# Optimization experiments

Hardware: AMD Instinct MI355X
Metric: run time of the kernel (lower is better)

The kernel has to match this reference:

```python
import jax, jax.numpy as jnp
import numpy as np

PRE_HEIGHT = 96
PRE_WIDTH = 128


def setup_inputs() -> dict:
    key = jax.random.key(0)
    B, K, H, W = 32, 64, 96, 128
    x = jax.random.normal(key, (B, K, H, W), dtype=jnp.float32)
    return {"combined_hm_preds": x, "batch_size": B, "num_of_kp": K}


def reference(combined_hm_preds, batch_size, num_of_kp):
    B, K, H, W = combined_hm_preds.shape
    # nn.Softmax() with no dim on a 4D tensor -> softmax over dim=1 (channels)
    map_val_all = jax.nn.softmax(combined_hm_preds, axis=1)
    # zeta[b,k] = sum over spatial of the channel-softmaxed map
    get_zeta = map_val_all.sum(axis=(2, 3))  # [B, K]
    js = jnp.arange(W, dtype=map_val_all.dtype)
    iis = jnp.arange(H, dtype=map_val_all.dtype)
    # per-channel weighted coordinate sums
    Sx = jnp.einsum('bkij,j->bk', map_val_all, js)  # [B, K]
    Sy = jnp.einsum('bkij,i->bk', map_val_all, iis)  # [B, K]
    # faithful to the original: accumulators are never reset across k or b,
    # so each keypoint uses the inclusive cumulative sum in flattened (b,k) order
    cum_x = jnp.cumsum(Sx.reshape(-1)).reshape(B, K)
    cum_y = jnp.cumsum(Sy.reshape(-1)).reshape(B, K)
    kx = jnp.round(cum_x / get_zeta)
    ky = jnp.round(cum_y / get_zeta)
    # out-of-range clamp to the image center, as in the original
    kx = jnp.where((kx > PRE_WIDTH) | (kx < 0), PRE_WIDTH * 0.5, kx)
    ky = jnp.where((ky > PRE_HEIGHT) | (ky < 0), PRE_HEIGHT * 0.5, ky)
    keypoint = jnp.stack([kx, ky], axis=-1)  # [B, K, 2]
    return (map_val_all, keypoint, get_zeta)
```

## Files before the change

### kernel.cpp

```cpp
#include <hip/hip_runtime.h>
#include <math.h>

#define BB 32
#define KK 64
#define HH 96
#define WW 128
#define HW (HH*WW)
#define MAP_SIZE (BB*KK*HW)
#define NBK (BB*KK)
#define NT  (HW/256)

__global__ __launch_bounds__(256) void fused_k(const float* __restrict__ x,
                                               float* __restrict__ out,
                                               double* __restrict__ sxyz) {
    __shared__ float  sm[KK][257];
    __shared__ float  dinv[256];
    __shared__ double pz[4][64], px[4][64], py[4][64];

    int blk  = blockIdx.x;
    int b    = blk / NT;
    int tile = blk - b * NT;
    int t    = threadIdx.x;
    size_t base = (size_t)b * KK * HW + (size_t)tile * 256 + t;

    float den = 0.f;
    #pragma unroll
    for (int k = 0; k < KK; ++k) {
        float e = __expf(x[base + (size_t)k * HW]);
        sm[k][t] = e;
        den += e;
    }
    float inv = 1.f / den;
    dinv[t] = inv;

    #pragma unroll
    for (int k = 0; k < KK; ++k) {
        out[base + (size_t)k * HW] = sm[k][t] * inv;
    }

    __syncthreads();

    int k = t & 63, chunk = t >> 6;
    int p0 = chunk * 64;
    double z = 0.0, sx = 0.0, sy = 0.0;
    #pragma unroll
    for (int j = 0; j < 64; ++j) {
        int p = p0 + j;
        double m = (double)(sm[k][p] * dinv[p]);
        int g = tile * 256 + p;
        z  += m;
        sx += m * (double)(g & (WW - 1));
        sy += m * (double)(g >> 7);
    }
    pz[chunk][k] = z; px[chunk][k] = sx; py[chunk][k] = sy;
    __syncthreads();

    if (t < 64) {
        double Z  = pz[0][t] + pz[1][t] + pz[2][t] + pz[3][t];
        double SX = px[0][t] + px[1][t] + px[2][t] + px[3][t];
        double SY = py[0][t] + py[1][t] + py[2][t] + py[3][t];
        int bk = b * KK + t;
        atomicAdd(&sxyz[bk * 3 + 0], SX);
        atomicAdd(&sxyz[bk * 3 + 1], SY);
        atomicAdd(&sxyz[bk * 3 + 2], Z);
    }
}

__global__ __launch_bounds__(256) void keypoint_k(const double* __restrict__ sxyz,
                                                  float* __restrict__ kp,
                                                  float* __restrict__ zeta) {
    const int PT = NBK / 256;
    int t = threadIdx.x;
    int lane = t & 63, wid = t >> 6;

    double vx[PT], vy[PT];
    double cx = 0.0, cy = 0.0;
    #pragma unroll
    for (int e = 0; e < PT; ++e) {
        int idx = t * PT + e;
        cx += sxyz[idx * 3 + 0]; vx[e] = cx;
        cy += sxyz[idx * 3 + 1]; vy[e] = cy;
    }
    double tx = cx, ty = cy;
    for (int off = 1; off < 64; off <<= 1) {
        double ax = __shfl_up(tx, off, 64);
        double ay = __shfl_up(ty, off, 64);
        if (lane >= off) { tx += ax; ty += ay; }
    }
    __shared__ double wxs[4], wys[4];
    if (lane == 63) { wxs[wid] = tx; wys[wid] = ty; }
    __syncthreads();
    double offx = tx - cx, offy = ty - cy;
    for (int w2 = 0; w2 < wid; ++w2) { offx += wxs[w2]; offy += wys[w2]; }

    #pragma unroll
    for (int e = 0; e < PT; ++e) {
        int idx = t * PT + e;
        double zz = sxyz[idx * 3 + 2];
        double kx = rint((vx[e] + offx) / zz);
        double ky = rint((vy[e] + offy) / zz);
        float fkx = (float)kx, fky = (float)ky;
        if (fkx > 128.0f || fkx < 0.0f) fkx = 64.0f;
        if (fky > 96.0f  || fky < 0.0f) fky = 48.0f;
        kp[idx * 2 + 0] = fkx;
        kp[idx * 2 + 1] = fky;
        zeta[idx] = (float)zz;
    }
}

extern "C" void kernel_launch(void* const* d_in, const int* in_sizes, int n_in,
                              void* d_out, int out_size, void* d_ws, size_t ws_size,
                              hipStream_t stream) {
    const float* x = (const float*)d_in[0];
    float* out  = (float*)d_out;
    float* map  = out;
    float* kp   = out + MAP_SIZE;
    float* zeta = out + MAP_SIZE + NBK * 2;
    double* sxyz = (double*)d_ws;

    hipMemsetAsync(d_ws, 0, (size_t)NBK * 3 * sizeof(double), stream);
    fused_k   <<< BB * NT, 256, 0, stream >>> (x, map, sxyz);
    keypoint_k<<< 1,       256, 0, stream >>> (sxyz, kp, zeta);
}
```

Measured before the change: 189.0 us.

## Chunk softmax reduction over channels, drop atomics for per-tile partials

The fused kernel now stores only 16-channel chunks in shared memory instead of all 64, recomputing exp on a second read of the input, which cuts LDS use and raises the occupancy hint to 4 blocks. The per-tile reductions run in float with a per-segment layout, and sy is derived from z because each segment lies within one image row. Double atomics are replaced by per-tile partial sums in a workspace, reduced by a new combine kernel. This trades a second read of the input and an extra launch, plus some float-precision risk, for less shared memory and no atomic contention.

```diff
diff --git a/kernel.cpp b/kernel.cpp
--- a/kernel.cpp
+++ b/kernel.cpp
@@ -9,13 +9,14 @@
 #define MAP_SIZE (BB*KK*HW)
 #define NBK (BB*KK)
 #define NT  (HW/256)
+#define CH  16
+#define NC  (KK/CH)
 
-__global__ __launch_bounds__(256) void fused_k(const float* __restrict__ x,
-                                               float* __restrict__ out,
-                                               double* __restrict__ sxyz) {
-    __shared__ float  sm[KK][257];
-    __shared__ float  dinv[256];
-    __shared__ double pz[4][64], px[4][64], py[4][64];
+__global__ __launch_bounds__(256, 4) void fused_k(const float* __restrict__ x,
+                                                  float* __restrict__ out,
+                                                  float* __restrict__ partial) {
+    __shared__ float sm[CH][257];
+    __shared__ float pacc[3][NC][CH][17];
 
     int blk  = blockIdx.x;
     int b    = blk / NT;
@@ -25,45 +26,73 @@
 
     float den = 0.f;
     #pragma unroll
-    for (int k = 0; k < KK; ++k) {
-        float e = __expf(x[base + (size_t)k * HW]);
-        sm[k][t] = e;
-        den += e;
-    }
+    for (int k = 0; k < KK; ++k)
+        den += __expf(x[base + (size_t)k * HW]);
     float inv = 1.f / den;
-    dinv[t] = inv;
+
+    int kin = t & 15, seg = t >> 4;
+    int i_img = tile * 2 + (seg >> 3);
+    float zc[NC], sxc[NC], syc[NC];
 
     #pragma unroll
-    for (int k = 0; k < KK; ++k) {
-        out[base + (size_t)k * HW] = sm[k][t] * inv;
+    for (int c = 0; c < NC; ++c) {
+        #pragma unroll
+        for (int kk2 = 0; kk2 < CH; ++kk2) {
+            int k = c * CH + kk2;
+            float m = __expf(x[base + (size_t)k * HW]) * inv;
+            out[base + (size_t)k * HW] = m;
+            sm[kk2][t] = m;
+        }
+        __syncthreads();
+        float z = 0.f, sx = 0.f;
+        #pragma unroll
+        for (int j = 0; j < 16; ++j) {
+            int p = seg * 16 + j;
+            float m = sm[kin][p];
+            z  += m;
+            sx += m * (float)(p & (WW - 1));
+        }
+        zc[c] = z; sxc[c] = sx; syc[c] = z * (float)i_img;
+        __syncthreads();
     }
 
+    #pragma unroll
+    for (int c = 0; c < NC; ++c) {
+        pacc[0][c][kin][seg] = zc[c];
+        pacc[1][c][kin][seg] = sxc[c];
+        pacc[2][c][kin][seg] = syc[c];
+    }
     __syncthreads();
+    if (t < KK) {
+        int c = t >> 4, k2 = t & 15;
+        double Z = 0.0, SX = 0.0, SY = 0.0;
+        #pragma unroll
+        for (int s2 = 0; s2 < 16; ++s2) {
+            Z  += (double)pacc[0][c][k2][s2];
+            SX += (double)pacc[1][c][k2][s2];
+            SY += (double)pacc[2][c][k2][s2];
+        }
+        int bk = b * KK + t;
+        size_t o = ((size_t)tile * NBK + bk) * 3;
+        partial[o + 0] = (float)SX;
+        partial[o + 1] = (float)SY;
+        partial[o + 2] = (float)Z;
+    }
+}
 
-    int k = t & 63, chunk = t >> 6;
-    int p0 = chunk * 64;
-    double z = 0.0, sx = 0.0, sy = 0.0;
-    #pragma unroll
-    for (int j = 0; j < 64; ++j) {
-        int p = p0 + j;
-        double m = (double)(sm[k][p] * dinv[p]);
-        int g = tile * 256 + p;
-        z  += m;
-        sx += m * (double)(g & (WW - 1));
-        sy += m * (double)(g >> 7);
+__global__ __launch_bounds__(64) void combine_k(const float* __restrict__ partial,
+                                                double* __restrict__ sxyz) {
+    int bk = blockIdx.x * 64 + threadIdx.x;
+    double SX = 0.0, SY = 0.0, Z = 0.0;
+    for (int tile = 0; tile < NT; ++tile) {
+        const float* p = partial + ((size_t)tile * NBK + bk) * 3;
+        SX += (double)p[0];
+        SY += (double)p[1];
+        Z  += (double)p[2];
     }
-    pz[chunk][k] = z; px[chunk][k] = sx; py[chunk][k] = sy;
-    __syncthreads();
-
-    if (t < 64) {
-        double Z  = pz[0][t] + pz[1][t] + pz[2][t] + pz[3][t];
-        double SX = px[0][t] + px[1][t] + px[2][t] + px[3][t];
-        double SY = py[0][t] + py[1][t] + py[2][t] + py[3][t];
-        int bk = b * KK + t;
-        atomicAdd(&sxyz[bk * 3 + 0], SX);
-        atomicAdd(&sxyz[bk * 3 + 1], SY);
-        atomicAdd(&sxyz[bk * 3 + 2], Z);
-    }
+    sxyz[bk * 3 + 0] = SX;
+    sxyz[bk * 3 + 1] = SY;
+    sxyz[bk * 3 + 2] = Z;
 }
 
 __global__ __launch_bounds__(256) void keypoint_k(const double* __restrict__ sxyz,
@@ -116,9 +145,12 @@
     float* map  = out;
     float* kp   = out + MAP_SIZE;
     float* zeta = out + MAP_SIZE + NBK * 2;
-    double* sxyz = (double*)d_ws;
 
-    hipMemsetAsync(d_ws, 0, (size_t)NBK * 3 * sizeof(double), stream);
-    fused_k   <<< BB * NT, 256, 0, stream >>> (x, map, sxyz);
-    keypoint_k<<< 1,       256, 0, stream >>> (sxyz, kp, zeta);
+    float*  partial = (float*)d_ws;
+    double* sxyz    = (double*)((char*)d_ws +
+                      ((size_t)NT * NBK * 3 * sizeof(float) + 255 & ~255ULL));
+
+    fused_k   <<< BB * NT, 256, 0, stream >>> (x, map, partial);
+    combine_k <<< NBK / 64, 64,  0, stream >>> (partial, sxyz);
+    keypoint_k<<< 1,        256, 0, stream >>> (sxyz, kp, zeta);
 }
```

After: 236.7 us. 1.25x slower.
